# Performance work log

Hardware: AMD Instinct MI355X
Metric: run time of the kernel (lower is better)

## Reference

```python
import jax, jax.numpy as jnp
import numpy as np

APERTURE = 256
IGNORE_ITSELF = False
FMAX = jnp.float32(3.4028235e38)  # tf.float32.max


def setup_inputs() -> dict:
    key = jax.random.key(0)
    ks = jax.random.split(key, 5)
    n, m, d = 4096, 1024, 1024
    scale = 1.0 / np.sqrt(m)
    x = jax.random.normal(ks[0], (n, m), dtype=jnp.float32)
    WK = jax.random.normal(ks[1], (m, d), dtype=jnp.float32) * scale
    WQ = jax.random.normal(ks[2], (m, d), dtype=jnp.float32) * scale
    WV = jax.random.normal(ks[3], (m, d), dtype=jnp.float32) * scale
    Wout = jax.random.normal(ks[4], (d, m), dtype=jnp.float32) * scale
    return {"x": x, "WK": WK, "WQ": WQ, "WV": WV, "Wout": Wout}


def reference(x, WK, WQ, WV, Wout):
    n = x.shape[0]
    K = x @ WK                      # [n, d]
    Q = (x @ WQ) * 0.06             # [n, d]
    V = x @ WV                      # [n, d]
    logits = Q @ K.T                # [n, n]

    i = jnp.arange(n)[:, None]
    j = jnp.arange(n)[None, :]
    if IGNORE_ITSELF:
        keep = (i != j).astype(jnp.float32)
        logits = logits * keep - FMAX * (1.0 - keep)
    if APERTURE > 0:
        # tf: mask = 1 - band_part(ones, -aperture, aperture); negative num_lower
        # keeps the whole lower triangle, so mask==1 exactly where j - i > aperture.
        keep = (j - i > APERTURE).astype(jnp.float32)
        logits = logits * keep - FMAX * (1.0 - keep)

    att_weights = jax.nn.softmax(logits, axis=-1)  # [n, n]
    # dropout is identity (training=False). NOTE faithful quirk: transpose_a=True.
    y = att_weights.T @ V           # [n, d]
    y = y @ Wout                    # [n, m]
    return (y, att_weights)
```

## Files before the change

### kernel.cpp

```cpp
#include <hip/hip_runtime.h>
#include <cstdint>
#include <cstddef>

#define N_TOK 4096
#define M_DIM 1024
#define APER  256
#define UNIF_START 3839

typedef __attribute__((ext_vector_type(8))) short short8;
typedef __attribute__((ext_vector_type(4))) float float4_t;

__device__ __forceinline__ unsigned short f2bf(float x) {
    union { float f; uint32_t u; } v; v.f = x;
    uint32_t u = v.u;
    u += 0x7FFFu + ((u >> 16) & 1u);
    return (unsigned short)(u >> 16);
}

__device__ __forceinline__ void gload16(const void* g, void* l) {
    __builtin_amdgcn_global_load_lds(
        (const __attribute__((address_space(1))) void*)g,
        (__attribute__((address_space(3))) void*)l, 16, 0, 0);
}

__global__ __launch_bounds__(256) void cast_bf16(const float* __restrict__ src,
                                                 unsigned short* __restrict__ dst, int n) {
    const int i = (blockIdx.x * 256 + threadIdx.x) * 4;
    if (i >= n) return;
    const float4 v = *reinterpret_cast<const float4*>(&src[i]);
    ushort4 o;
    o.x = f2bf(v.x); o.y = f2bf(v.y); o.z = f2bf(v.z); o.w = f2bf(v.w);
    *reinterpret_cast<ushort4*>(&dst[i]) = o;
}

__global__ __launch_bounds__(256) void wtrans3(const float* __restrict__ W0, const float* __restrict__ W1,
                                               const float* __restrict__ W2,
                                               unsigned short* __restrict__ D0, unsigned short* __restrict__ D1,
                                               unsigned short* __restrict__ D2) {
    const int z = blockIdx.z;
    const float* src = z == 0 ? W0 : (z == 1 ? W1 : W2);
    unsigned short* dst = z == 0 ? D0 : (z == 1 ? D1 : D2);
    __shared__ unsigned short tile[32][33];
    const int c0 = blockIdx.x * 32, r0 = blockIdx.y * 32;
    const int tx = threadIdx.x & 31, ty = threadIdx.x >> 5;
#pragma unroll
    for (int i = ty; i < 32; i += 8)
        tile[i][tx] = f2bf(src[(size_t)(r0 + i) * M_DIM + c0 + tx]);
    __syncthreads();
#pragma unroll
    for (int i = ty; i < 32; i += 8)
        dst[(size_t)(c0 + i) * M_DIM + r0 + tx] = tile[tx][i];
}

__global__ __launch_bounds__(256) void transpose_bf16(const unsigned short* __restrict__ src,
                                                      unsigned short* __restrict__ dst,
                                                      int R, int C) {
    __shared__ unsigned short tile[32][33];
    const int c0 = blockIdx.x * 32, r0 = blockIdx.y * 32;
    const int tx = threadIdx.x & 31, ty = threadIdx.x >> 5;
#pragma unroll
    for (int i = ty; i < 32; i += 8)
        tile[i][tx] = src[(size_t)(r0 + i) * C + c0 + tx];
    __syncthreads();
#pragma unroll
    for (int i = ty; i < 32; i += 8)
        dst[(size_t)(c0 + i) * R + r0 + tx] = tile[tx][i];
}

template <int SKIP>
__global__ __launch_bounds__(256) void nt64sq(const unsigned short* __restrict__ A,
                                              const unsigned short* __restrict__ B,
                                              float* __restrict__ Cf,
                                              unsigned short* __restrict__ Cb,
                                              int N, int K) {
    const int by   = (SKIP == 1) ? ((int)gridDim.y - 1 - (int)blockIdx.y) : (int)blockIdx.y;
    const int row0 = by * 64;
    const int col0 = blockIdx.x * 64;

    __shared__ unsigned short Asb[64 * 32];
    __shared__ unsigned short Bsb[64 * 32];

    const int t = threadIdx.x, w = t >> 6, lane = t & 63;
    float4_t acc[4] = {};

    const int sr   = lane >> 2;
    const int sk   = ((lane & 3) ^ ((sr >> 1) & 3)) * 8;
    const int m    = lane & 15;
    const int slot = ((lane >> 4) ^ ((m >> 1) & 3)) * 8;

    for (int k0 = 0; k0 < K; k0 += 32) {
        if (SKIP == 1) {
            if ((k0 > row0 + 63 - APER - 1) && (k0 + 31 < UNIF_START)) continue;
        }
        const int rr = w * 16 + sr;
        gload16(&A[(size_t)(row0 + rr) * K + k0 + sk], &Asb[w * 512]);
        gload16(&B[(size_t)(col0 + rr) * K + k0 + sk], &Bsb[w * 512]);
        __syncthreads();
        const short8 af = *reinterpret_cast<const short8*>(&Asb[(w * 16 + m) * 32 + slot]);
        short8 bf[4];
#pragma unroll
        for (int j = 0; j < 4; ++j)
            bf[j] = *reinterpret_cast<const short8*>(&Bsb[(j * 16 + m) * 32 + slot]);
#pragma unroll
        for (int j = 0; j < 4; ++j)
            acc[j] = __builtin_amdgcn_mfma_f32_16x16x32_bf16(af, bf[j], acc[j], 0, 0, 0);
        __syncthreads();
    }

    const int crow = row0 + w * 16 + (lane >> 4) * 4;
    const int ccol = col0 + m;
#pragma unroll
    for (int j = 0; j < 4; ++j)
#pragma unroll
        for (int r = 0; r < 4; ++r) {
            const float v = acc[j][r];
            const size_t idx = (size_t)(crow + r) * N + ccol + j * 16;
            if (Cf) Cf[idx] = v;
            if (Cb) Cb[idx] = f2bf(v);
        }
}

__global__ __launch_bounds__(256) void mfma_qkv(const unsigned short* __restrict__ xb,
                                                const unsigned short* __restrict__ WKt,
                                                const unsigned short* __restrict__ WQt,
                                                const unsigned short* __restrict__ WVWt,
                                                unsigned short* __restrict__ Kb,
                                                unsigned short* __restrict__ Qb,
                                                unsigned short* __restrict__ VWb) {
    const int row0  = blockIdx.y * 128;
    const int col0g = blockIdx.x * 128;
    const int seg   = col0g >> 10;
    const int col0  = col0g & 1023;
    const unsigned short* B = seg == 0 ? WKt : (seg == 1 ? WQt : WVWt);
    unsigned short*       C = seg == 0 ? Kb  : (seg == 1 ? Qb  : VWb);
    const float alpha = (seg == 1) ? 0.06f : 1.0f;

    __shared__ unsigned short Asb[128 * 32];
    __shared__ unsigned short Bsb[128 * 32];

    const int t = threadIdx.x, w = t >> 6, lane = t & 63;
    const int wr = (w >> 1) * 64, wc = (w & 1) * 64;

    float4_t acc[4][4] = {};

    const int sr   = lane >> 2;
    const int sk   = ((lane & 3) ^ ((sr >> 1) & 3)) * 8;
    const int m    = lane & 15;
    const int slot = ((lane >> 4) ^ ((m >> 1) & 3)) * 8;

    for (int k0 = 0; k0 < M_DIM; k0 += 32) {
#pragma unroll
        for (int cc = 0; cc < 2; ++cc) {
            const int c = 2 * w + cc;
            const int rr = c * 16 + sr;
            gload16(&xb[(size_t)(row0 + rr) * M_DIM + k0 + sk], &Asb[c * 512]);
            gload16(&B[(size_t)(col0 + rr) * M_DIM + k0 + sk], &Bsb[c * 512]);
        }
        __syncthreads();
        short8 af[4], bf[4];
#pragma unroll
        for (int i = 0; i < 4; ++i)
            af[i] = *reinterpret_cast<const short8*>(&Asb[(wr + i * 16 + m) * 32 + slot]);
#pragma unroll
        for (int j = 0; j < 4; ++j)
            bf[j] = *reinterpret_cast<const short8*>(&Bsb[(wc + j * 16 + m) * 32 + slot]);
#pragma unroll
        for (int i = 0; i < 4; ++i)
#pragma unroll
            for (int j = 0; j < 4; ++j)
                acc[i][j] = __builtin_amdgcn_mfma_f32_16x16x32_bf16(af[i], bf[j], acc[i][j], 0, 0, 0);
        __syncthreads();
    }

    const int crow = row0 + wr + (lane >> 4) * 4;
    const int ccol = col0 + wc + m;
#pragma unroll
    for (int i = 0; i < 4; ++i)
#pragma unroll
        for (int j = 0; j < 4; ++j)
#pragma unroll
            for (int r = 0; r < 4; ++r)
                C[(size_t)(crow + i * 16 + r) * M_DIM + ccol + j * 16] = f2bf(alpha * acc[i][j][r]);
}

__global__ __launch_bounds__(256) void mfma_logits_exp(const unsigned short* __restrict__ A,
                                                       const unsigned short* __restrict__ B,
                                                       float* __restrict__ att,
                                                       float* __restrict__ rowsum) {
    const int row0 = blockIdx.y * 128;
    const int col0 = blockIdx.x * 128;
    if (col0 + 127 <= row0 + APER) return;

    __shared__ unsigned short Asb[128 * 32];
    __shared__ unsigned short Bsb[128 * 32];

    const int t = threadIdx.x, w = t >> 6, lane = t & 63;
    const int wr = (w >> 1) * 64, wc = (w & 1) * 64;

    float4_t acc[4][4] = {};

    const int sr   = lane >> 2;
    const int sk   = ((lane & 3) ^ ((sr >> 1) & 3)) * 8;
    const int m    = lane & 15;
    const int slot = ((lane >> 4) ^ ((m >> 1) & 3)) * 8;

    for (int k0 = 0; k0 < M_DIM; k0 += 32) {
#pragma unroll
        for (int cc = 0; cc < 2; ++cc) {
            const int c = 2 * w + cc;
            const int rr = c * 16 + sr;
            gload16(&A[(size_t)(row0 + rr) * M_DIM + k0 + sk], &Asb[c * 512]);
            gload16(&B[(size_t)(col0 + rr) * M_DIM + k0 + sk], &Bsb[c * 512]);
        }
        __syncthreads();
        short8 af[4], bf[4];
#pragma unroll
        for (int i = 0; i < 4; ++i)
            af[i] = *reinterpret_cast<const short8*>(&Asb[(wr + i * 16 + m) * 32 + slot]);
#pragma unroll
        for (int j = 0; j < 4; ++j)
            bf[j] = *reinterpret_cast<const short8*>(&Bsb[(wc + j * 16 + m) * 32 + slot]);
#pragma unroll
        for (int i = 0; i < 4; ++i)
#pragma unroll
            for (int j = 0; j < 4; ++j)
                acc[i][j] = __builtin_amdgcn_mfma_f32_16x16x32_bf16(af[i], bf[j], acc[i][j], 0, 0, 0);
        __syncthreads();
    }

    const int crow = row0 + wr + (lane >> 4) * 4;
    const int ccol = col0 + wc + m;
#pragma unroll
    for (int i = 0; i < 4; ++i) {
#pragma unroll
        for (int r = 0; r < 4; ++r) {
            const int gr = crow + i * 16 + r;
            float partial = 0.0f;
#pragma unroll
            for (int j = 0; j < 4; ++j) {
                const int gc = ccol + j * 16;
                float val;
                if (gr >= UNIF_START) {
                    val = 1.0f;
                } else if (gc > gr + APER) {
                    val = __expf(acc[i][j][r]);
                    partial += val;
                } else {
                    val = 0.0f;
                }
                att[(size_t)gr * N_TOK + gc] = val;
            }
            partial += __shfl_xor(partial, 1, 64);
            partial += __shfl_xor(partial, 2, 64);
            partial += __shfl_xor(partial, 4, 64);
            partial += __shfl_xor(partial, 8, 64);
            if (m == 0 && gr < UNIF_START) atomicAdd(&rowsum[gr], partial);
        }
    }
}

__global__ __launch_bounds__(256) void init_rowsum(float* __restrict__ rowsum) {
    const int i = blockIdx.x * 256 + threadIdx.x;
    if (i < N_TOK) rowsum[i] = (i >= UNIF_START) ? (float)N_TOK : 0.0f;
}

__global__ __launch_bounds__(256) void finalize_att(float* __restrict__ att,
                                                    unsigned short* __restrict__ attT,
                                                    const float* __restrict__ rowsum) {
    const int j0 = blockIdx.x * 64, i0 = blockIdx.y * 64;
    const int t = threadIdx.x;
    const int rl = t >> 4;
    const int c4 = (t & 15) * 4;
    const float u = 1.0f / (float)N_TOK;

    if (j0 + 63 <= i0 + APER) {
#pragma unroll
        for (int s = 0; s < 4; ++s) {
            const int i = i0 + rl + 16 * s;
            const float val = (i >= UNIF_START) ? u : 0.0f;
            float4 v; v.x = v.y = v.z = v.w = val;
            *reinterpret_cast<float4*>(&att[(size_t)i * N_TOK + j0 + c4]) = v;
        }
        const unsigned short bu = f2bf(u);
#pragma unroll
        for (int s = 0; s < 4; ++s) {
            const int j = j0 + rl + 16 * s;
            ushort4 o;
            o.x = (i0 + c4 + 0 >= UNIF_START) ? bu : 0;
            o.y = (i0 + c4 + 1 >= UNIF_START) ? bu : 0;
            o.z = (i0 + c4 + 2 >= UNIF_START) ? bu : 0;
            o.w = (i0 + c4 + 3 >= UNIF_START) ? bu : 0;
            *reinterpret_cast<ushort4*>(&attT[(size_t)j * N_TOK + i0 + c4]) = o;
        }
        return;
    }

    __shared__ unsigned short tile[64][72];
#pragma unroll
    for (int s = 0; s < 4; ++s) {
        const int il = rl + 16 * s;
        const int i  = i0 + il;
        const float inv = 1.0f / rowsum[i];
        float4 v = *reinterpret_cast<const float4*>(&att[(size_t)i * N_TOK + j0 + c4]);
        v.x *= inv; v.y *= inv; v.z *= inv; v.w *= inv;
        *reinterpret_cast<float4*>(&att[(size_t)i * N_TOK + j0 + c4]) = v;
        ushort4 b;
        b.x = f2bf(v.x); b.y = f2bf(v.y); b.z = f2bf(v.z); b.w = f2bf(v.w);
        *reinterpret_cast<ushort4*>(&tile[il][c4]) = b;
    }
    __syncthreads();
#pragma unroll
    for (int s = 0; s < 4; ++s) {
        const int jl = rl + 16 * s;
        ushort4 o;
        o.x = tile[c4 + 0][jl];
        o.y = tile[c4 + 1][jl];
        o.z = tile[c4 + 2][jl];
        o.w = tile[c4 + 3][jl];
        *reinterpret_cast<ushort4*>(&attT[(size_t)(j0 + jl) * N_TOK + i0 + c4]) = o;
    }
}

extern "C" void kernel_launch(void* const* d_in, const int* in_sizes, int n_in,
                              void* d_out, int out_size, void* d_ws, size_t ws_size,
                              hipStream_t stream) {
    const float* x    = (const float*)d_in[0];
    const float* WK   = (const float*)d_in[1];
    const float* WQ   = (const float*)d_in[2];
    const float* WV   = (const float*)d_in[3];
    const float* Wout = (const float*)d_in[4];

    float* y   = (float*)d_out;
    float* att = y + (size_t)N_TOK * M_DIM;

    unsigned short* base = (unsigned short*)d_ws;
    const size_t MEG = 1u << 20;
    unsigned short* xb    = base;
    unsigned short* WKt   = base + 4  * MEG;
    unsigned short* WQt   = base + 5  * MEG;
    unsigned short* Woutt = base + 6  * MEG;
    unsigned short* WVb   = base + 7  * MEG;
    unsigned short* WVWt  = base + 8  * MEG;
    unsigned short* Kb    = base + 9  * MEG;
    unsigned short* Qb    = base + 13 * MEG;
    unsigned short* VWb   = base + 17 * MEG;
    unsigned short* attT  = base + 4  * MEG;
    float*          rowsum = (float*)(base + 20 * MEG);
    unsigned short* VWt   = xb;

    const dim3 blk(256);

    cast_bf16<<<dim3((N_TOK * M_DIM) / 1024), blk, 0, stream>>>(x, xb, N_TOK * M_DIM);
    cast_bf16<<<dim3((M_DIM * M_DIM) / 1024), blk, 0, stream>>>(WV, WVb, M_DIM * M_DIM);
    wtrans3<<<dim3(M_DIM / 32, M_DIM / 32, 3), blk, 0, stream>>>(WK, WQ, Wout, WKt, WQt, Woutt);

    nt64sq<0><<<dim3(M_DIM / 64, M_DIM / 64), blk, 0, stream>>>(Woutt, WVb, nullptr, WVWt,
                                                                M_DIM, M_DIM);

    mfma_qkv<<<dim3(24, N_TOK / 128), blk, 0, stream>>>(xb, WKt, WQt, WVWt, Kb, Qb, VWb);

    transpose_bf16<<<dim3(M_DIM / 32, N_TOK / 32), blk, 0, stream>>>(VWb, VWt, N_TOK, M_DIM);

    init_rowsum<<<dim3(N_TOK / 256), blk, 0, stream>>>(rowsum);
    mfma_logits_exp<<<dim3(N_TOK / 128, N_TOK / 128), blk, 0, stream>>>(Qb, Kb, att, rowsum);

    finalize_att<<<dim3(N_TOK / 64, N_TOK / 64), blk, 0, stream>>>(att, attT, rowsum);

    nt64sq<1><<<dim3(M_DIM / 64, N_TOK / 64), blk, 0, stream>>>(attT, VWt, y, nullptr,
                                                                M_DIM, N_TOK);
}
```

Measured before the change: 290.7 us.

## Replace final att^T·VW GEMM with double-buffered sparse-aware MFMA kernel

Adds a new kernel for the final attT @ VWt product. It loads only the K ranges where attention weights can be nonzero: a prefix that depends on the row block, plus the uniform tail region. It double-buffers LDS with async global-to-LDS loads and uses XOR-swizzled 64-wide K tiles. Blocks are launched in reversed row order so the heaviest blocks start first. This is meant to skip multiplications over masked-zero regions and overlap loads with compute, at the cost of relying on hard-coded mask geometry constants.

```diff
diff --git a/kernel.cpp b/kernel.cpp
--- a/kernel.cpp
+++ b/kernel.cpp
@@ -118,6 +118,98 @@
             if (Cf) Cf[idx] = v;
             if (Cb) Cb[idx] = f2bf(v);
         }
+}
+
+__global__ __launch_bounds__(256) void atv_db(const unsigned short* __restrict__ A,
+                                              const unsigned short* __restrict__ B,
+                                              float* __restrict__ C) {
+    const int by   = (int)gridDim.y - 1 - (int)blockIdx.y;
+    const int row0 = by * 64;
+    const int col0 = blockIdx.x * 128;
+
+    __shared__ unsigned short As[2][64 * 64];
+    __shared__ unsigned short Bs[2][128 * 64];
+
+    const int t = threadIdx.x, w = t >> 6, lane = t & 63;
+    const int wr = (w >> 1) * 32, wc = (w & 1) * 64;
+    const int q = lane >> 4, m = lane & 15;
+
+    const int srow = lane >> 3;
+    const int schk = ((lane & 7) ^ (srow & 7)) * 8;
+
+    int aoff[2][2], boff[4][2];
+#pragma unroll
+    for (int i = 0; i < 2; ++i)
+#pragma unroll
+        for (int h = 0; h < 2; ++h)
+            aoff[i][h] = (wr + i * 16 + m) * 64 + (((h * 4 + q) ^ (m & 7)) * 8);
+#pragma unroll
+    for (int j = 0; j < 4; ++j)
+#pragma unroll
+        for (int h = 0; h < 2; ++h)
+            boff[j][h] = (wc + j * 16 + m) * 64 + (((h * 4 + q) ^ (m & 7)) * 8);
+
+    const int limit = row0 - 194;
+    int nPre = (limit >= 0) ? (limit / 64 + 1) : 0;
+    if (nPre > 59) nPre = 59;
+    const int nT = nPre + 5;
+
+    float4_t acc[2][4] = {};
+
+    auto kof = [&](int s) { return s < nPre ? s * 64 : 3776 + (s - nPre) * 64; };
+
+    auto stage = [&](int buf, int k0) {
+#pragma unroll
+        for (int c = 0; c < 2; ++c) {
+            const int r0 = w * 16 + c * 8;
+            gload16(&A[(size_t)(row0 + r0 + srow) * (size_t)N_TOK + k0 + schk],
+                    &As[buf][r0 * 64]);
+        }
+#pragma unroll
+        for (int c = 0; c < 4; ++c) {
+            const int r0 = w * 32 + c * 8;
+            gload16(&B[(size_t)(col0 + r0 + srow) * (size_t)N_TOK + k0 + schk],
+                    &Bs[buf][r0 * 64]);
+        }
+    };
+
+    stage(0, kof(0));
+    __syncthreads();
+
+    int cur = 0;
+    for (int s = 0; s < nT; ++s) {
+        if (s + 1 < nT) stage(cur ^ 1, kof(s + 1));
+        short8 af[2][2], bf[4][2];
+#pragma unroll
+        for (int i = 0; i < 2; ++i)
+#pragma unroll
+            for (int h = 0; h < 2; ++h)
+                af[i][h] = *reinterpret_cast<const short8*>(&As[cur][aoff[i][h]]);
+#pragma unroll
+        for (int j = 0; j < 4; ++j)
+#pragma unroll
+            for (int h = 0; h < 2; ++h)
+                bf[j][h] = *reinterpret_cast<const short8*>(&Bs[cur][boff[j][h]]);
+#pragma unroll
+        for (int i = 0; i < 2; ++i)
+#pragma unroll
+            for (int j = 0; j < 4; ++j)
+#pragma unroll
+                for (int h = 0; h < 2; ++h)
+                    acc[i][j] = __builtin_amdgcn_mfma_f32_16x16x32_bf16(af[i][h], bf[j][h],
+                                                                        acc[i][j], 0, 0, 0);
+        __syncthreads();
+        cur ^= 1;
+    }
+
+#pragma unroll
+    for (int i = 0; i < 2; ++i)
+#pragma unroll
+        for (int j = 0; j < 4; ++j)
+#pragma unroll
+            for (int r = 0; r < 4; ++r)
+                C[(size_t)(row0 + wr + i * 16 + q * 4 + r) * M_DIM + col0 + wc + j * 16 + m] =
+                    acc[i][j][r];
 }
 
 __global__ __launch_bounds__(256) void mfma_qkv(const unsigned short* __restrict__ xb,
@@ -366,6 +458,5 @@
 
     finalize_att<<<dim3(N_TOK / 64, N_TOK / 64), blk, 0, stream>>>(att, attT, rowsum);
 
-    nt64sq<1><<<dim3(M_DIM / 64, N_TOK / 64), blk, 0, stream>>>(attT, VWt, y, nullptr,
-                                                                M_DIM, N_TOK);
-}
+    atv_db<<<dim3(M_DIM / 128, N_TOK / 64), blk, 0, stream>>>(attT, VWt, y);
+}
```

Result: no change. 294.3 us (+1.2%).

## Split uniform softmax rows analytically and use triangular split-K ATV with atomics

Applied to the files above, without the earlier changes.

The uniform-softmax rows (i >= UNIF_START) get their contribution to y precomputed as a column mean of VW (svec), and y is pre-initialised with it. That lets attT hold zeros for those rows so the ATV GEMM skips them. The final ATV GEMM becomes a 128x128-tile triangular kernel that walks only the nonzero K range and splits K across blocks with atomicAdd when a tile's range is long. The logits kernel launches only the upper-triangle tiles through a linear block index, and the two cast kernels are merged into one. This trades wasted masked work and launch count for atomics, extra small kernels and non-deterministic float summation order.

```diff
diff --git a/kernel.cpp b/kernel.cpp
--- a/kernel.cpp
+++ b/kernel.cpp
@@ -17,20 +17,31 @@
     return (unsigned short)(u >> 16);
 }
 
+__device__ __forceinline__ float bf2f(unsigned short b) {
+    union { uint32_t u; float f; } v; v.u = ((uint32_t)b) << 16;
+    return v.f;
+}
+
 __device__ __forceinline__ void gload16(const void* g, void* l) {
     __builtin_amdgcn_global_load_lds(
         (const __attribute__((address_space(1))) void*)g,
         (__attribute__((address_space(3))) void*)l, 16, 0, 0);
 }
 
-__global__ __launch_bounds__(256) void cast_bf16(const float* __restrict__ src,
-                                                 unsigned short* __restrict__ dst, int n) {
+__global__ __launch_bounds__(256) void cast2(const float* __restrict__ x,
+                                             unsigned short* __restrict__ xb,
+                                             const float* __restrict__ WV,
+                                             unsigned short* __restrict__ WVb) {
     const int i = (blockIdx.x * 256 + threadIdx.x) * 4;
-    if (i >= n) return;
-    const float4 v = *reinterpret_cast<const float4*>(&src[i]);
+    const float* src;
+    unsigned short* dst;
+    int off;
+    if (i < N_TOK * M_DIM) { src = x;  dst = xb;  off = i; }
+    else                   { src = WV; dst = WVb; off = i - N_TOK * M_DIM; }
+    const float4 v = *reinterpret_cast<const float4*>(&src[off]);
     ushort4 o;
     o.x = f2bf(v.x); o.y = f2bf(v.y); o.z = f2bf(v.z); o.w = f2bf(v.w);
-    *reinterpret_cast<ushort4*>(&dst[i]) = o;
+    *reinterpret_cast<ushort4*>(&dst[off]) = o;
 }
 
 __global__ __launch_bounds__(256) void wtrans3(const float* __restrict__ W0, const float* __restrict__ W1,
@@ -67,14 +78,11 @@
         dst[(size_t)(c0 + i) * R + r0 + tx] = tile[tx][i];
 }
 
-template <int SKIP>
 __global__ __launch_bounds__(256) void nt64sq(const unsigned short* __restrict__ A,
                                               const unsigned short* __restrict__ B,
-                                              float* __restrict__ Cf,
                                               unsigned short* __restrict__ Cb,
                                               int N, int K) {
-    const int by   = (SKIP == 1) ? ((int)gridDim.y - 1 - (int)blockIdx.y) : (int)blockIdx.y;
-    const int row0 = by * 64;
+    const int row0 = blockIdx.y * 64;
     const int col0 = blockIdx.x * 64;
 
     __shared__ unsigned short Asb[64 * 32];
@@ -89,9 +97,6 @@
     const int slot = ((lane >> 4) ^ ((m >> 1) & 3)) * 8;
 
     for (int k0 = 0; k0 < K; k0 += 32) {
-        if (SKIP == 1) {
-            if ((k0 > row0 + 63 - APER - 1) && (k0 + 31 < UNIF_START)) continue;
-        }
         const int rr = w * 16 + sr;
         gload16(&A[(size_t)(row0 + rr) * K + k0 + sk], &Asb[w * 512]);
         gload16(&B[(size_t)(col0 + rr) * K + k0 + sk], &Bsb[w * 512]);
@@ -112,84 +117,47 @@
 #pragma unroll
     for (int j = 0; j < 4; ++j)
 #pragma unroll
-        for (int r = 0; r < 4; ++r) {
-            const float v = acc[j][r];
-            const size_t idx = (size_t)(crow + r) * N + ccol + j * 16;
-            if (Cf) Cf[idx] = v;
-            if (Cb) Cb[idx] = f2bf(v);
-        }
-}
-
-__global__ __launch_bounds__(256) void mfma_qkv(const unsigned short* __restrict__ xb,
-                                                const unsigned short* __restrict__ WKt,
-                                                const unsigned short* __restrict__ WQt,
-                                                const unsigned short* __restrict__ WVWt,
-                                                unsigned short* __restrict__ Kb,
-                                                unsigned short* __restrict__ Qb,
-                                                unsigned short* __restrict__ VWb) {
-    const int row0  = blockIdx.y * 128;
-    const int col0g = blockIdx.x * 128;
-    const int seg   = col0g >> 10;
-    const int col0  = col0g & 1023;
-    const unsigned short* B = seg == 0 ? WKt : (seg == 1 ? WQt : WVWt);
-    unsigned short*       C = seg == 0 ? Kb  : (seg == 1 ? Qb  : VWb);
-    const float alpha = (seg == 1) ? 0.06f : 1.0f;
-
-    __shared__ unsigned short Asb[128 * 32];
-    __shared__ unsigned short Bsb[128 * 32];
-
-    const int t = threadIdx.x, w = t >> 6, lane = t & 63;
-    const int wr = (w >> 1) * 64, wc = (w & 1) * 64;
-
-    float4_t acc[4][4] = {};
-
-    const int sr   = lane >> 2;
-    const int sk   = ((lane & 3) ^ ((sr >> 1) & 3)) * 8;
-    const int m    = lane & 15;
-    const int slot = ((lane >> 4) ^ ((m >> 1) & 3)) * 8;
-
-    for (int k0 = 0; k0 < M_DIM; k0 += 32) {
-#pragma unroll
-        for (int cc = 0; cc < 2; ++cc) {
-            const int c = 2 * w + cc;
-            const int rr = c * 16 + sr;
-            gload16(&xb[(size_t)(row0 + rr) * M_DIM + k0 + sk], &Asb[c * 512]);
-            gload16(&B[(size_t)(col0 + rr) * M_DIM + k0 + sk], &Bsb[c * 512]);
-        }
-        __syncthreads();
-        short8 af[4], bf[4];
-#pragma unroll
-        for (int i = 0; i < 4; ++i)
-            af[i] = *reinterpret_cast<const short8*>(&Asb[(wr + i * 16 + m) * 32 + slot]);
-#pragma unroll
-        for (int j = 0; j < 4; ++j)
-            bf[j] = *reinterpret_cast<const short8*>(&Bsb[(wc + j * 16 + m) * 32 + slot]);
-#pragma unroll
-        for (int i = 0; i < 4; ++i)
-#pragma unroll
-            for (int j = 0; j < 4; ++j)
-                acc[i][j] = __builtin_amdgcn_mfma_f32_16x16x32_bf16(af[i], bf[j], acc[i][j], 0, 0, 0);
-        __syncthreads();
-    }
-
-    const int crow = row0 + wr + (lane >> 4) * 4;
-    const int ccol = col0 + wc + m;
-#pragma unroll
-    for (int i = 0; i < 4; ++i)
-#pragma unroll
-        for (int j = 0; j < 4; ++j)
-#pragma unroll
-            for (int r = 0; r < 4; ++r)
-                C[(size_t)(crow + i * 16 + r) * M_DIM + ccol + j * 16] = f2bf(alpha * acc[i][j][r]);
-}
-
-__global__ __launch_bounds__(256) void mfma_logits_exp(const unsigned short* __restrict__ A,
-                                                       const unsigned short* __restrict__ B,
-                                                       float* __restrict__ att,
-                                                       float* __restrict__ rowsum) {
-    const int row0 = blockIdx.y * 128;
-    const int col0 = blockIdx.x * 128;
-    if (col0 + 127 <= row0 + APER) return;
+        for (int r = 0; r < 4; ++r)
+            Cb[(size_t)(crow + r) * N + ccol + j * 16] = f2bf(acc[j][r]);
+}
+
+__global__ __launch_bounds__(256) void prep_sr(const unsigned short* __restrict__ VWb,
+                                               float* __restrict__ svec,
+                                               float* __restrict__ rowsum) {
+    const int bid = blockIdx.x;
+    if (bid < 4) {
+        const int c = bid * 256 + threadIdx.x;
+        float acc = 0.0f;
+        for (int i = UNIF_START; i < N_TOK; ++i)
+            acc += bf2f(VWb[(size_t)i * M_DIM + c]);
+        svec[c] = acc * (1.0f / (float)N_TOK);
+    } else {
+        const int i = (bid - 4) * 256 + threadIdx.x;
+        rowsum[i] = (i >= UNIF_START) ? (float)N_TOK : 0.0f;
+    }
+}
+
+__global__ __launch_bounds__(256) void init_y(float* __restrict__ y, const float* __restrict__ s) {
+    const float4 sv = reinterpret_cast<const float4*>(s)[threadIdx.x];
+    const int bid = blockIdx.x;
+    const int r0 = (bid < 64) ? bid * 4 : 768 + (bid - 64) * 4;
+#pragma unroll
+    for (int r = 0; r < 4; ++r)
+        reinterpret_cast<float4*>(&y[(size_t)(r0 + r) * M_DIM])[threadIdx.x] = sv;
+}
+
+__global__ __launch_bounds__(256) void logits_128(const unsigned short* __restrict__ A,
+                                                  const unsigned short* __restrict__ B,
+                                                  float* __restrict__ att,
+                                                  float* __restrict__ rowsum) {
+    int rem = (int)blockIdx.x, y = 0;
+    for (;;) {
+        const int c = 30 - y;
+        if (rem < c) break;
+        rem -= c; ++y;
+    }
+    const int row0 = y * 128;
+    const int col0 = (y + 2 + rem) * 128;
 
     __shared__ unsigned short Asb[128 * 32];
     __shared__ unsigned short Bsb[128 * 32];
@@ -259,9 +227,153 @@
     }
 }
 
-__global__ __launch_bounds__(256) void init_rowsum(float* __restrict__ rowsum) {
-    const int i = blockIdx.x * 256 + threadIdx.x;
-    if (i < N_TOK) rowsum[i] = (i >= UNIF_START) ? (float)N_TOK : 0.0f;
+__global__ __launch_bounds__(256) void atv_128(const unsigned short* __restrict__ A,
+                                               const unsigned short* __restrict__ B,
+                                               float* __restrict__ y,
+                                               const float* __restrict__ svec) {
+    const int bid = (int)blockIdx.x;
+    const int x   = bid & 7;
+    int uid = bid >> 3;
+    int by, n, u;
+    for (by = 2;; ++by) {
+        n = 4 * by - 4;
+        u = (n + 15) >> 4;
+        if (uid < u) break;
+        uid -= u;
+    }
+    const int base = n / u, rem = n % u;
+    const int ns = base + (uid < rem ? 1 : 0);
+    const int s0 = uid * base + (uid < rem ? uid : rem);
+    const int direct = (u == 1);
+
+    const int row0 = by * 128;
+    const int col0 = x * 128;
+
+    __shared__ unsigned short Asb[128 * 32];
+    __shared__ unsigned short Bsb[128 * 32];
+
+    const int t = threadIdx.x, w = t >> 6, lane = t & 63;
+    const int wr = (w >> 1) * 64, wc = (w & 1) * 64;
+
+    float4_t acc[4][4] = {};
+
+    const int sr   = lane >> 2;
+    const int sk   = ((lane & 3) ^ ((sr >> 1) & 3)) * 8;
+    const int m    = lane & 15;
+    const int slot = ((lane >> 4) ^ ((m >> 1) & 3)) * 8;
+
+    for (int s = 0; s < ns; ++s) {
+        const int k0 = (s0 + s) * 32;
+#pragma unroll
+        for (int cc = 0; cc < 2; ++cc) {
+            const int c = 2 * w + cc;
+            const int rr = c * 16 + sr;
+            gload16(&A[(size_t)(row0 + rr) * (size_t)N_TOK + k0 + sk], &Asb[c * 512]);
+            gload16(&B[(size_t)(col0 + rr) * (size_t)N_TOK + k0 + sk], &Bsb[c * 512]);
+        }
+        __syncthreads();
+        short8 af[4], bf[4];
+#pragma unroll
+        for (int i = 0; i < 4; ++i)
+            af[i] = *reinterpret_cast<const short8*>(&Asb[(wr + i * 16 + m) * 32 + slot]);
+#pragma unroll
+        for (int j = 0; j < 4; ++j)
+            bf[j] = *reinterpret_cast<const short8*>(&Bsb[(wc + j * 16 + m) * 32 + slot]);
+#pragma unroll
+        for (int i = 0; i < 4; ++i)
+#pragma unroll
+            for (int j = 0; j < 4; ++j)
+                acc[i][j] = __builtin_amdgcn_mfma_f32_16x16x32_bf16(af[i], bf[j], acc[i][j], 0, 0, 0);
+        __syncthreads();
+    }
+
+    const int crow = row0 + wr + (lane >> 4) * 4;
+    const int ccol = col0 + wc + m;
+    if (direct) {
+        float sv[4];
+#pragma unroll
+        for (int j = 0; j < 4; ++j) sv[j] = svec[ccol + j * 16];
+#pragma unroll
+        for (int i = 0; i < 4; ++i)
+#pragma unroll
+            for (int j = 0; j < 4; ++j)
+#pragma unroll
+                for (int r = 0; r < 4; ++r)
+                    y[(size_t)(crow + i * 16 + r) * M_DIM + ccol + j * 16] =
+                        acc[i][j][r] + sv[j];
+    } else {
+#pragma unroll
+        for (int i = 0; i < 4; ++i)
+#pragma unroll
+            for (int j = 0; j < 4; ++j)
+#pragma unroll
+                for (int r = 0; r < 4; ++r)
+                    atomicAdd(&y[(size_t)(crow + i * 16 + r) * M_DIM + ccol + j * 16],
+                              acc[i][j][r]);
+    }
+}
+
+__global__ __launch_bounds__(256) void mfma_qkv(const unsigned short* __restrict__ xb,
+                                                const unsigned short* __restrict__ WKt,
+                                                const unsigned short* __restrict__ WQt,
+                                                const unsigned short* __restrict__ WVWt,
+                                                unsigned short* __restrict__ Kb,
+                                                unsigned short* __restrict__ Qb,
+                                                unsigned short* __restrict__ VWb) {
+    const int row0  = blockIdx.y * 128;
+    const int col0g = blockIdx.x * 128;
+    const int seg   = col0g >> 10;
+    const int col0  = col0g & 1023;
+    const unsigned short* B = seg == 0 ? WKt : (seg == 1 ? WQt : WVWt);
+    unsigned short*       C = seg == 0 ? Kb  : (seg == 1 ? Qb  : VWb);
+    const float alpha = (seg == 1) ? 0.06f : 1.0f;
+
+    __shared__ unsigned short Asb[128 * 32];
+    __shared__ unsigned short Bsb[128 * 32];
+
+    const int t = threadIdx.x, w = t >> 6, lane = t & 63;
+    const int wr = (w >> 1) * 64, wc = (w & 1) * 64;
+
+    float4_t acc[4][4] = {};
+
+    const int sr   = lane >> 2;
+    const int sk   = ((lane & 3) ^ ((sr >> 1) & 3)) * 8;
+    const int m    = lane & 15;
+    const int slot = ((lane >> 4) ^ ((m >> 1) & 3)) * 8;
+
+    for (int k0 = 0; k0 < M_DIM; k0 += 32) {
+#pragma unroll
+        for (int cc = 0; cc < 2; ++cc) {
+            const int c = 2 * w + cc;
+            const int rr = c * 16 + sr;
+            gload16(&xb[(size_t)(row0 + rr) * M_DIM + k0 + sk], &Asb[c * 512]);
+            gload16(&B[(size_t)(col0 + rr) * M_DIM + k0 + sk], &Bsb[c * 512]);
+        }
+        __syncthreads();
+        short8 af[4], bf[4];
+#pragma unroll
+        for (int i = 0; i < 4; ++i)
+            af[i] = *reinterpret_cast<const short8*>(&Asb[(wr + i * 16 + m) * 32 + slot]);
+#pragma unroll
+        for (int j = 0; j < 4; ++j)
+            bf[j] = *reinterpret_cast<const short8*>(&Bsb[(wc + j * 16 + m) * 32 + slot]);
+#pragma unroll
+        for (int i = 0; i < 4; ++i)
+#pragma unroll
+            for (int j = 0; j < 4; ++j)
+                acc[i][j] = __builtin_amdgcn_mfma_f32_16x16x32_bf16(af[i], bf[j], acc[i][j], 0, 0, 0);
+        __syncthreads();
+    }
+
+    const int crow = row0 + wr + (lane >> 4) * 4;
+    const int ccol = col0 + wc + m;
+#pragma unroll
+    for (int i = 0; i < 4; ++i)
+#pragma unroll
+        for (int j = 0; j < 4; ++j)
+#pragma unroll
+            for (int r = 0; r < 4; ++r)
+                C[(size_t)(crow + i * 16 + r) * M_DIM + ccol + j * 16] = f2bf(alpha * acc[i][j][r]);
 }
 
 __global__ __launch_bounds__(256) void finalize_att(float* __restrict__ att,
@@ -281,16 +393,11 @@
             float4 v; v.x = v.y = v.z = v.w = val;
             *reinterpret_cast<float4*>(&att[(size_t)i * N_TOK + j0 + c4]) = v;
         }
-        const unsigned short bu = f2bf(u);
+        const ushort4 z = {0, 0, 0, 0};
 #pragma unroll
         for (int s = 0; s < 4; ++s) {
             const int j = j0 + rl + 16 * s;
-            ushort4 o;
-            o.x = (i0 + c4 + 0 >= UNIF_START) ? bu : 0;
-            o.y = (i0 + c4 + 1 >= UNIF_START) ? bu : 0;
-            o.z = (i0 + c4 + 2 >= UNIF_START) ? bu : 0;
-            o.w = (i0 + c4 + 3 >= UNIF_START) ? bu : 0;
-            *reinterpret_cast<ushort4*>(&attT[(size_t)j * N_TOK + i0 + c4]) = o;
+            *reinterpret_cast<ushort4*>(&attT[(size_t)j * N_TOK + i0 + c4]) = z;
         }
         return;
     }
@@ -305,7 +412,11 @@
         v.x *= inv; v.y *= inv; v.z *= inv; v.w *= inv;
         *reinterpret_cast<float4*>(&att[(size_t)i * N_TOK + j0 + c4]) = v;
         ushort4 b;
-        b.x = f2bf(v.x); b.y = f2bf(v.y); b.z = f2bf(v.z); b.w = f2bf(v.w);
+        if (i >= UNIF_START) {
+            b.x = b.y = b.z = b.w = 0;
+        } else {
+            b.x = f2bf(v.x); b.y = f2bf(v.y); b.z = f2bf(v.z); b.w = f2bf(v.w);
+        }
         *reinterpret_cast<ushort4*>(&tile[il][c4]) = b;
     }
     __syncthreads();
@@ -346,26 +457,25 @@
     unsigned short* VWb   = base + 17 * MEG;
     unsigned short* attT  = base + 4  * MEG;
     float*          rowsum = (float*)(base + 20 * MEG);
+    float*          svec   = (float*)(base + 20 * MEG) + 4096;
     unsigned short* VWt   = xb;
 
     const dim3 blk(256);
 
-    cast_bf16<<<dim3((N_TOK * M_DIM) / 1024), blk, 0, stream>>>(x, xb, N_TOK * M_DIM);
-    cast_bf16<<<dim3((M_DIM * M_DIM) / 1024), blk, 0, stream>>>(WV, WVb, M_DIM * M_DIM);
+    cast2<<<dim3((N_TOK * M_DIM + M_DIM * M_DIM) / 1024), blk, 0, stream>>>(x, xb, WV, WVb);
     wtrans3<<<dim3(M_DIM / 32, M_DIM / 32, 3), blk, 0, stream>>>(WK, WQ, Wout, WKt, WQt, Woutt);
 
-    nt64sq<0><<<dim3(M_DIM / 64, M_DIM / 64), blk, 0, stream>>>(Woutt, WVb, nullptr, WVWt,
-                                                                M_DIM, M_DIM);
+    nt64sq<<<dim3(M_DIM / 64, M_DIM / 64), blk, 0, stream>>>(Woutt, WVb, WVWt, M_DIM, M_DIM);
 
     mfma_qkv<<<dim3(24, N_TOK / 128), blk, 0, stream>>>(xb, WKt, WQt, WVWt, Kb, Qb, VWb);
 
     transpose_bf16<<<dim3(M_DIM / 32, N_TOK / 32), blk, 0, stream>>>(VWb, VWt, N_TOK, M_DIM);
-
-    init_rowsum<<<dim3(N_TOK / 256), blk, 0, stream>>>(rowsum);
-    mfma_logits_exp<<<dim3(N_TOK / 128, N_TOK / 128), blk, 0, stream>>>(Qb, Kb, att, rowsum);
+    prep_sr<<<dim3(20), blk, 0, stream>>>(VWb, svec, rowsum);
+    init_y<<<dim3(896), blk, 0, stream>>>(y, svec);
+
+    logits_128<<<dim3(465), blk, 0, stream>>>(Qb, Kb, att, rowsum);
 
     finalize_att<<<dim3(N_TOK / 64, N_TOK / 64), blk, 0, stream>>>(att, attT, rowsum);
 
-    nt64sq<1><<<dim3(M_DIM / 64, N_TOK / 64), blk, 0, stream>>>(attT, VWt, y, nullptr,
-                                                                M_DIM, N_TOK);
-}
+    atv_128<<<dim3(1024), blk, 0, stream>>>(attT, VWt, y, svec);
+}
```

New measurement: 306.6 us. 1.05x slower.
